# Kernel optimization log

Measured on AMD Instinct MI355X. Metric: run time of the kernel, lower is better.

Reference implementation:

```python
import jax, jax.numpy as jnp
import numpy as np

B, T, D_IN, H, D_OUT = 64, 512, 256, 512, 1


def _lstm_layer(x, w_ih, w_hh, b_ih, b_hh):
    """PyTorch-convention LSTM layer. x: [B,T,Din]; w_ih: [4H,Din]; w_hh: [4H,H].
    Gate order: i, f, g, o. Zero initial h/c. Returns [B,T,H]."""
    h_dim = w_hh.shape[1]
    # Precompute input contribution for all timesteps: [B,T,4H]
    xg = jnp.einsum('bti,gi->btg', x, w_ih) + b_ih + b_hh
    xg = jnp.swapaxes(xg, 0, 1)  # [T,B,4H] for scan

    def step(carry, xg_t):
        h, c = carry
        gates = xg_t + h @ w_hh.T  # [B,4H]
        i, f, g, o = jnp.split(gates, 4, axis=-1)
        i = jax.nn.sigmoid(i)
        f = jax.nn.sigmoid(f)
        g = jnp.tanh(g)
        o = jax.nn.sigmoid(o)
        c = f * c + i * g
        h = o * jnp.tanh(c)
        return (h, c), h

    bsz = x.shape[0]
    h0 = jnp.zeros((bsz, h_dim), dtype=x.dtype)
    c0 = jnp.zeros((bsz, h_dim), dtype=x.dtype)
    _, hs = jax.lax.scan(step, (h0, c0), xg)  # hs: [T,B,H]
    return jnp.swapaxes(hs, 0, 1)  # [B,T,H]


def setup_inputs() -> dict:
    key = jax.random.key(0)
    ks = jax.random.split(key, 11)
    s_ih0 = 1.0 / np.sqrt(H)
    inp = {
        'x': jax.random.normal(ks[0], (B, T, D_IN), dtype=jnp.float32),
        'w_ih0': jax.random.uniform(ks[1], (4 * H, D_IN), jnp.float32, -s_ih0, s_ih0),
        'w_hh0': jax.random.uniform(ks[2], (4 * H, H), jnp.float32, -s_ih0, s_ih0),
        'b_ih0': jax.random.uniform(ks[3], (4 * H,), jnp.float32, -s_ih0, s_ih0),
        'b_hh0': jax.random.uniform(ks[4], (4 * H,), jnp.float32, -s_ih0, s_ih0),
        'w_ih1': jax.random.uniform(ks[5], (4 * H, H), jnp.float32, -s_ih0, s_ih0),
        'w_hh1': jax.random.uniform(ks[6], (4 * H, H), jnp.float32, -s_ih0, s_ih0),
        'b_ih1': jax.random.uniform(ks[7], (4 * H,), jnp.float32, -s_ih0, s_ih0),
        'b_hh1': jax.random.uniform(ks[8], (4 * H,), jnp.float32, -s_ih0, s_ih0),
        'w_fc': jax.random.uniform(ks[9], (D_OUT, H), jnp.float32, -s_ih0, s_ih0),
        'b_fc': jax.random.uniform(ks[10], (D_OUT,), jnp.float32, -s_ih0, s_ih0),
    }
    return inp


def reference(x, w_ih0, w_hh0, b_ih0, b_hh0, w_ih1, w_hh1, b_ih1, b_hh1, w_fc, b_fc):
    h = _lstm_layer(x, w_ih0, w_hh0, b_ih0, b_hh0)   # [B,T,H]
    h = _lstm_layer(h, w_ih1, w_hh1, b_ih1, b_hh1)   # [B,T,H]
    last = h[:, -1, :]                               # [B,H]
    logits = last @ w_fc.T + b_fc                    # [B,D_OUT]
    return jax.nn.sigmoid(logits)
```

## Files before the change

kernel.cpp:

```cpp
#include <hip/hip_runtime.h>
#include <stdint.h>
#include <stddef.h>

#define B_ 64
#define T_ 512
#define DIN 256
#define H_ 512
#define NWGF 256

typedef __attribute__((ext_vector_type(8))) short short8;
typedef __attribute__((ext_vector_type(4))) float f32x4;

__device__ __forceinline__ unsigned short f2bf(float f) {
  union { float f; unsigned u; } v; v.f = f;
  return (unsigned short)((v.u + 0x7fffu + ((v.u >> 16) & 1u)) >> 16);
}
__device__ __forceinline__ float bf2f(unsigned short s) {
  union { unsigned u; float f; } v; v.u = ((unsigned)s) << 16; return v.f;
}
__device__ __forceinline__ float sigmoidf_(float x) { return 1.f / (1.f + __expf(-x)); }
__device__ __forceinline__ float tanhf_(float x) { return 1.f - 2.f / (__expf(2.f * x) + 1.f); }

__device__ __forceinline__ void cohstore_u64(unsigned long long* p, unsigned long long v) {
  __hip_atomic_store(p, v, __ATOMIC_RELAXED, __HIP_MEMORY_SCOPE_AGENT);
}
__device__ __forceinline__ int cohload_i32(const int* p) {
  return __hip_atomic_load(p, __ATOMIC_RELAXED, __HIP_MEMORY_SCOPE_AGENT);
}
__device__ __forceinline__ void cohstore_i32(int* p, int v) {
  __hip_atomic_store(p, v, __ATOMIC_RELAXED, __HIP_MEMORY_SCOPE_AGENT);
}

__global__ void k_convert_x(const float* __restrict__ x, unsigned short* __restrict__ xT) {
  const int nq = T_ * B_ * DIN / 4;
  for (int q = blockIdx.x * blockDim.x + threadIdx.x; q < nq; q += gridDim.x * blockDim.x) {
    int e = q * 4;
    int d = e % DIN;
    int row = e / DIN;
    int b = row & (B_ - 1), t = row / B_;
    float4 v = *(const float4*)(x + ((size_t)b * T_ + t) * DIN + d);
    unsigned short o[4] = { f2bf(v.x), f2bf(v.y), f2bf(v.z), f2bf(v.w) };
    *(uint2*)(xT + (size_t)row * DIN + d) = *(const uint2*)o;
  }
}

__global__ __launch_bounds__(256, 1) void k_lstm9(
    const unsigned short* __restrict__ xT,
    const float* __restrict__ wih0, const float* __restrict__ whh0,
    const float* __restrict__ bih0, const float* __restrict__ bhh0,
    const float* __restrict__ wih1, const float* __restrict__ whh1,
    const float* __restrict__ bih1, const float* __restrict__ bhh1,
    unsigned short* __restrict__ h0, unsigned short* __restrict__ h1,
    int* __restrict__ flg) {
  __shared__ unsigned short hbufA[8192];
  __shared__ unsigned short bufB[8192];
  __shared__ float gbuf[4 * 64 * 5];
  __shared__ unsigned short hstage[16 * 20];
  const int bid = blockIdx.x;
  const int grp = bid & 7, cg = bid >> 3;
  const int layer = grp >> 2, bq = grp & 3;
  const int tid = threadIdx.x;
  const int lane = tid & 63, wv = tid >> 6;
  const int l15 = lane & 15, l4 = lane >> 4;
  const int colb = cg * 16, bb = bq * 16;
  const int ucol = tid & 15, ubat = tid >> 4;
  const int lp = (ubat >> 2) * 16 + ucol, ur = ubat & 3;
  int* myflag = flg + (grp * 32 + cg) * 32;
  const int* f_own = flg + (grp * 32) * 32;
  const int* f_l0  = flg + (bq * 32) * 32;

  if (layer == 0) {
    short8 wih[8], whh[16];
    {
      const float* wr = wih0 + (size_t)(wv * H_ + colb + l15) * DIN + l4 * 8;
#pragma unroll
      for (int kk = 0; kk < 8; ++kk) {
        float4 v0 = *(const float4*)(wr + kk * 32);
        float4 v1 = *(const float4*)(wr + kk * 32 + 4);
        unsigned short o[8] = { f2bf(v0.x), f2bf(v0.y), f2bf(v0.z), f2bf(v0.w),
                                f2bf(v1.x), f2bf(v1.y), f2bf(v1.z), f2bf(v1.w) };
        wih[kk] = *(const short8*)o;
      }
      const float* wr2 = whh0 + (size_t)(wv * H_ + colb + l15) * H_ + l4 * 8;
#pragma unroll
      for (int kk = 0; kk < 16; ++kk) {
        float4 v0 = *(const float4*)(wr2 + kk * 32);
        float4 v1 = *(const float4*)(wr2 + kk * 32 + 4);
        unsigned short o[8] = { f2bf(v0.x), f2bf(v0.y), f2bf(v0.z), f2bf(v0.w),
                                f2bf(v1.x), f2bf(v1.y), f2bf(v1.z), f2bf(v1.w) };
        whh[kk] = *(const short8*)o;
      }
    }
    float b0s[4];
#pragma unroll
    for (int s = 0; s < 4; ++s)
      b0s[s] = bih0[s * H_ + colb + ucol] + bhh0[s * H_ + colb + ucol];
    float cst = 0.f;

#pragma unroll
    for (int j = 0; j < 2; ++j) {
      int ch = tid + j * 256;
      int b = ch >> 5, g = ch & 31;
      uint4 v = *(const uint4*)(xT + (size_t)(bb + b) * DIN + g * 8);
      *(uint4*)&bufB[g * 128 + ((b ^ (g & 15)) * 8)] = v;
    }
    __syncthreads();

    for (int t = 0; t < T_; ++t) {
      f32x4 aE = {}, aO = {};
      {
        const unsigned short* xb = bufB + (t & 1) * 4096;
#pragma unroll
        for (int kk = 0; kk < 8; kk += 2) {
          int g0 = kk * 4 + l4, g1 = (kk + 1) * 4 + l4;
          short8 a0 = *(const short8*)&xb[g0 * 128 + ((l15 ^ (g0 & 15)) * 8)];
          short8 a1 = *(const short8*)&xb[g1 * 128 + ((l15 ^ (g1 & 15)) * 8)];
          aE = __builtin_amdgcn_mfma_f32_16x16x32_bf16(a0, wih[kk], aE, 0, 0, 0);
          aO = __builtin_amdgcn_mfma_f32_16x16x32_bf16(a1, wih[kk + 1], aO, 0, 0, 0);
        }
      }
      uint4 xv[2];
      const bool hasx = (t + 1 < T_);
      if (hasx) {
        const unsigned short* xs = xT + (size_t)(t + 1) * (B_ * DIN);
#pragma unroll
        for (int j = 0; j < 2; ++j) {
          int ch = tid + j * 256;
          xv[j] = *(const uint4*)(xs + (size_t)(bb + (ch >> 5)) * DIN + (ch & 31) * 8);
        }
      }
      if (t > 0) {
        for (;;) {
          int v = (lane < 32) ? cohload_i32(f_own + lane * 32) : 0x7fffffff;
          if (__all(v >= t)) break;
          __builtin_amdgcn_s_sleep(1);
        }
        __builtin_amdgcn_sched_barrier(0);
        asm volatile("" ::: "memory");
        const uint4* hp = (const uint4*)(h0 + ((size_t)(t - 1) * B_ + bb) * H_);
        uint4 tmp[4];
#pragma unroll
        for (int j = 0; j < 4; ++j) tmp[j] = hp[tid + j * 256];
#pragma unroll
        for (int j = 0; j < 4; ++j) {
          int ch = tid + j * 256;
          int b = ch >> 6, g = ch & 63;
          *(uint4*)&hbufA[g * 128 + ((b ^ (g & 15)) * 8)] = tmp[j];
        }
      }
      if (hasx) {
        unsigned short* xd = bufB + ((t + 1) & 1) * 4096;
#pragma unroll
        for (int j = 0; j < 2; ++j) {
          int ch = tid + j * 256;
          int b = ch >> 5, g = ch & 31;
          *(uint4*)&xd[g * 128 + ((b ^ (g & 15)) * 8)] = xv[j];
        }
      }
      __syncthreads();
      if (t > 0) {
#pragma unroll
        for (int kk = 0; kk < 16; kk += 2) {
          int g0 = kk * 4 + l4, g1 = (kk + 1) * 4 + l4;
          short8 a0 = *(const short8*)&hbufA[g0 * 128 + ((l15 ^ (g0 & 15)) * 8)];
          short8 a1 = *(const short8*)&hbufA[g1 * 128 + ((l15 ^ (g1 & 15)) * 8)];
          aE = __builtin_amdgcn_mfma_f32_16x16x32_bf16(a0, whh[kk], aE, 0, 0, 0);
          aO = __builtin_amdgcn_mfma_f32_16x16x32_bf16(a1, whh[kk + 1], aO, 0, 0, 0);
        }
      }
      f32x4 acc = aE + aO;
#pragma unroll
      for (int r = 0; r < 4; ++r) gbuf[(wv * 64 + lane) * 5 + r] = acc[r];
      __syncthreads();
      {
        float g4[4];
#pragma unroll
        for (int s = 0; s < 4; ++s) g4[s] = gbuf[(s * 64 + lp) * 5 + ur] + b0s[s];
        float iv = sigmoidf_(g4[0]), fv = sigmoidf_(g4[1]);
        float gv = tanhf_(g4[2]), ov = sigmoidf_(g4[3]);
        cst = fv * cst + iv * gv;
        hstage[ubat * 20 + ucol] = f2bf(ov * tanhf_(cst));
      }
      __syncthreads();
      if (tid < 64) {
        int bl = tid >> 2, q = tid & 3;
        unsigned long long v = *(const unsigned long long*)&hstage[bl * 20 + q * 4];
        cohstore_u64((unsigned long long*)(h0 + ((size_t)t * B_ + bb + bl) * H_ + colb) + q, v);
      }
      asm volatile("s_waitcnt vmcnt(0)" ::: "memory");
      __syncthreads();
      if (tid == 0) cohstore_i32(myflag, t + 1);
    }
  } else {
    short8 wA[16], wB[16];
    {
      const float* wrA = wih1 + (size_t)(wv * H_ + colb + l15) * H_ + l4 * 8;
      const float* wrB = whh1 + (size_t)(wv * H_ + colb + l15) * H_ + l4 * 8;
#pragma unroll
      for (int kk = 0; kk < 16; ++kk) {
        float4 a0 = *(const float4*)(wrA + kk * 32);
        float4 a1 = *(const float4*)(wrA + kk * 32 + 4);
        unsigned short oa[8] = { f2bf(a0.x), f2bf(a0.y), f2bf(a0.z), f2bf(a0.w),
                                 f2bf(a1.x), f2bf(a1.y), f2bf(a1.z), f2bf(a1.w) };
        wA[kk] = *(const short8*)oa;
        float4 b0 = *(const float4*)(wrB + kk * 32);
        float4 b1 = *(const float4*)(wrB + kk * 32 + 4);
        unsigned short ob[8] = { f2bf(b0.x), f2bf(b0.y), f2bf(b0.z), f2bf(b0.w),
                                 f2bf(b1.x), f2bf(b1.y), f2bf(b1.z), f2bf(b1.w) };
        wB[kk] = *(const short8*)ob;
      }
    }
    float b1s[4];
#pragma unroll
    for (int s = 0; s < 4; ++s)
      b1s[s] = bih1[s * H_ + colb + ucol] + bhh1[s * H_ + colb + ucol];
    float cst = 0.f;

    for (int t = 0; t < T_; ++t) {
      for (;;) {
        int v = (lane < 32) ? cohload_i32(f_l0 + lane * 32) : 0x7fffffff;
        if (__all(v >= t + 1)) break;
        __builtin_amdgcn_s_sleep(1);
      }
      __builtin_amdgcn_sched_barrier(0);
      asm volatile("" ::: "memory");
      uint4 ha[4];
      {
        const uint4* hp = (const uint4*)(h0 + ((size_t)t * B_ + bb) * H_);
#pragma unroll
        for (int j = 0; j < 4; ++j) ha[j] = hp[tid + j * 256];
      }
      if (t > 0) {
        for (;;) {
          int v = (lane < 32) ? cohload_i32(f_own + lane * 32) : 0x7fffffff;
          if (__all(v >= t)) break;
          __builtin_amdgcn_s_sleep(1);
        }
        __builtin_amdgcn_sched_barrier(0);
        asm volatile("" ::: "memory");
        const uint4* hp = (const uint4*)(h1 + ((size_t)(t - 1) * B_ + bb) * H_);
        uint4 hbv[4];
#pragma unroll
        for (int j = 0; j < 4; ++j) hbv[j] = hp[tid + j * 256];
#pragma unroll
        for (int j = 0; j < 4; ++j) {
          int ch = tid + j * 256;
          int b = ch >> 6, g = ch & 63;
          *(uint4*)&bufB[g * 128 + ((b ^ (g & 15)) * 8)] = hbv[j];
        }
      }
      __syncthreads();
      f32x4 bE = {}, bO = {};
      if (t > 0) {
#pragma unroll
        for (int kk = 0; kk < 16; kk += 2) {
          int g0 = kk * 4 + l4, g1 = (kk + 1) * 4 + l4;
          short8 a0 = *(const short8*)&bufB[g0 * 128 + ((l15 ^ (g0 & 15)) * 8)];
          short8 a1 = *(const short8*)&bufB[g1 * 128 + ((l15 ^ (g1 & 15)) * 8)];
          bE = __builtin_amdgcn_mfma_f32_16x16x32_bf16(a0, wB[kk], bE, 0, 0, 0);
          bO = __builtin_amdgcn_mfma_f32_16x16x32_bf16(a1, wB[kk + 1], bO, 0, 0, 0);
        }
      }
#pragma unroll
      for (int j = 0; j < 4; ++j) {
        int ch = tid + j * 256;
        int b = ch >> 6, g = ch & 63;
        *(uint4*)&hbufA[g * 128 + ((b ^ (g & 15)) * 8)] = ha[j];
      }
      __syncthreads();
      f32x4 aE = {}, aO = {};
#pragma unroll
      for (int kk = 0; kk < 16; kk += 2) {
        int g0 = kk * 4 + l4, g1 = (kk + 1) * 4 + l4;
        short8 a0 = *(const short8*)&hbufA[g0 * 128 + ((l15 ^ (g0 & 15)) * 8)];
        short8 a1 = *(const short8*)&hbufA[g1 * 128 + ((l15 ^ (g1 & 15)) * 8)];
        aE = __builtin_amdgcn_mfma_f32_16x16x32_bf16(a0, wA[kk], aE, 0, 0, 0);
        aO = __builtin_amdgcn_mfma_f32_16x16x32_bf16(a1, wA[kk + 1], aO, 0, 0, 0);
      }
      f32x4 acc = (aE + aO) + (bE + bO);
#pragma unroll
      for (int r = 0; r < 4; ++r) gbuf[(wv * 64 + lane) * 5 + r] = acc[r];
      __syncthreads();
      {
        float g4[4];
#pragma unroll
        for (int s = 0; s < 4; ++s) g4[s] = gbuf[(s * 64 + lp) * 5 + ur] + b1s[s];
        float iv = sigmoidf_(g4[0]), fv = sigmoidf_(g4[1]);
        float gv = tanhf_(g4[2]), ov = sigmoidf_(g4[3]);
        cst = fv * cst + iv * gv;
        hstage[ubat * 20 + ucol] = f2bf(ov * tanhf_(cst));
      }
      __syncthreads();
      if (tid < 64) {
        int bl = tid >> 2, q = tid & 3;
        unsigned long long v = *(const unsigned long long*)&hstage[bl * 20 + q * 4];
        cohstore_u64((unsigned long long*)(h1 + ((size_t)t * B_ + bb + bl) * H_ + colb) + q, v);
      }
      asm volatile("s_waitcnt vmcnt(0)" ::: "memory");
      __syncthreads();
      if (tid == 0) cohstore_i32(myflag, t + 1);
    }
  }
}

__global__ void k_fc(const unsigned short* __restrict__ h1, const float* __restrict__ w,
                     const float* __restrict__ bfc, float* __restrict__ out) {
  int b = threadIdx.x;
  if (b < B_) {
    const unsigned short* hb = h1 + ((size_t)(T_ - 1) * B_ + b) * H_;
    float s = 0.f;
    for (int j = 0; j < H_; ++j) s += bf2f(hb[j]) * w[j];
    out[b] = sigmoidf_(s + bfc[0]);
  }
}

extern "C" void kernel_launch(void* const* d_in, const int* in_sizes, int n_in,
                              void* d_out, int out_size, void* d_ws, size_t ws_size,
                              hipStream_t stream) {
  (void)in_sizes; (void)n_in; (void)out_size; (void)ws_size;
  const float* x    = (const float*)d_in[0];
  const float* wih0 = (const float*)d_in[1];
  const float* whh0 = (const float*)d_in[2];
  const float* bih0 = (const float*)d_in[3];
  const float* bhh0 = (const float*)d_in[4];
  const float* wih1 = (const float*)d_in[5];
  const float* whh1 = (const float*)d_in[6];
  const float* bih1 = (const float*)d_in[7];
  const float* bhh1 = (const float*)d_in[8];
  const float* wfc  = (const float*)d_in[9];
  const float* bfc  = (const float*)d_in[10];
  float* out = (float*)d_out;

  const size_t HB = (size_t)T_ * B_ * H_ * 2;
  char* ws = (char*)d_ws;
  int* flg = (int*)ws;
  unsigned short* h0 = (unsigned short*)(ws + 32768);
  unsigned short* h1 = (unsigned short*)(ws + 32768 + HB);
  unsigned short* xT = (unsigned short*)(ws + 32768 + 2 * HB);

  hipMemsetAsync(ws, 0, 32768, stream);
  k_convert_x<<<2048, 256, 0, stream>>>(x, xT);
  k_lstm9<<<NWGF, 256, 0, stream>>>(xT, wih0, whh0, bih0, bhh0,
                                    wih1, whh1, bih1, bhh1, h0, h1, flg);
  k_fc<<<1, 64, 0, stream>>>(h1, wfc, bfc, out);
}
```

Before: 1.842 ms.

## Stage hidden tiles via direct global-to-LDS loads and trim per-step barriers

The per-timestep hidden-state tiles are now copied with global_load_lds straight into the swizzled shared buffers, replacing the load-to-register-then-store path. The h output is written directly from each lane with a shuffle-packed 32-bit store, which removes the hstage buffer and one __syncthreads per step. The flag spin loops no longer sleep, and layer 1 now waits on both flag sets in a single combined poll and issues both matmuls after one barrier. This shortens the serial critical path of each recurrent step, at the cost of busier polling traffic and reliance on the swizzled LDS addressing being correct for the direct-to-LDS writes.

```diff
diff --git a/kernel.cpp b/kernel.cpp
--- a/kernel.cpp
+++ b/kernel.cpp
@@ -11,6 +11,9 @@
 typedef __attribute__((ext_vector_type(8))) short short8;
 typedef __attribute__((ext_vector_type(4))) float f32x4;
 
+typedef const __attribute__((address_space(1))) unsigned int* gas_ptr;
+typedef __attribute__((address_space(3))) unsigned int* las_ptr;
+
 __device__ __forceinline__ unsigned short f2bf(float f) {
   union { float f; unsigned u; } v; v.f = f;
   return (unsigned short)((v.u + 0x7fffu + ((v.u >> 16) & 1u)) >> 16);
@@ -21,7 +24,7 @@
 __device__ __forceinline__ float sigmoidf_(float x) { return 1.f / (1.f + __expf(-x)); }
 __device__ __forceinline__ float tanhf_(float x) { return 1.f - 2.f / (__expf(2.f * x) + 1.f); }
 
-__device__ __forceinline__ void cohstore_u64(unsigned long long* p, unsigned long long v) {
+__device__ __forceinline__ void cohstore_u32(unsigned* p, unsigned v) {
   __hip_atomic_store(p, v, __ATOMIC_RELAXED, __HIP_MEMORY_SCOPE_AGENT);
 }
 __device__ __forceinline__ int cohload_i32(const int* p) {
@@ -29,6 +32,21 @@
 }
 __device__ __forceinline__ void cohstore_i32(int* p, int v) {
   __hip_atomic_store(p, v, __ATOMIC_RELAXED, __HIP_MEMORY_SCOPE_AGENT);
+}
+
+__device__ __forceinline__ void gload_lds16(const void* g, void* l) {
+  __builtin_amdgcn_global_load_lds((gas_ptr)g, (las_ptr)l, 16, 0, 0);
+}
+
+__device__ __forceinline__ void stage_tile_gl(const unsigned short* __restrict__ src,
+                                              unsigned short* __restrict__ dst, int tid) {
+#pragma unroll
+  for (int j = 0; j < 4; ++j) {
+    int u = tid + j * 256;
+    int g = u >> 4, b = (u & 15) ^ (g & 15);
+    gload_lds16(src + (size_t)b * H_ + g * 8,
+                dst + (size_t)((tid & ~63) + j * 256) * 8);
+  }
 }
 
 __global__ void k_convert_x(const float* __restrict__ x, unsigned short* __restrict__ xT) {
@@ -44,7 +62,7 @@
   }
 }
 
-__global__ __launch_bounds__(256, 1) void k_lstm9(
+__global__ __launch_bounds__(256, 1) void k_lstm10(
     const unsigned short* __restrict__ xT,
     const float* __restrict__ wih0, const float* __restrict__ whh0,
     const float* __restrict__ bih0, const float* __restrict__ bhh0,
@@ -55,7 +73,6 @@
   __shared__ unsigned short hbufA[8192];
   __shared__ unsigned short bufB[8192];
   __shared__ float gbuf[4 * 64 * 5];
-  __shared__ unsigned short hstage[16 * 20];
   const int bid = blockIdx.x;
   const int grp = bid & 7, cg = bid >> 3;
   const int layer = grp >> 2, bq = grp & 3;
@@ -133,20 +150,10 @@
         for (;;) {
           int v = (lane < 32) ? cohload_i32(f_own + lane * 32) : 0x7fffffff;
           if (__all(v >= t)) break;
-          __builtin_amdgcn_s_sleep(1);
         }
         __builtin_amdgcn_sched_barrier(0);
         asm volatile("" ::: "memory");
-        const uint4* hp = (const uint4*)(h0 + ((size_t)(t - 1) * B_ + bb) * H_);
-        uint4 tmp[4];
-#pragma unroll
-        for (int j = 0; j < 4; ++j) tmp[j] = hp[tid + j * 256];
-#pragma unroll
-        for (int j = 0; j < 4; ++j) {
-          int ch = tid + j * 256;
-          int b = ch >> 6, g = ch & 63;
-          *(uint4*)&hbufA[g * 128 + ((b ^ (g & 15)) * 8)] = tmp[j];
-        }
+        stage_tile_gl(h0 + ((size_t)(t - 1) * B_ + bb) * H_, hbufA, tid);
       }
       if (hasx) {
         unsigned short* xd = bufB + ((t + 1) & 1) * 4096;
@@ -179,13 +186,10 @@
         float iv = sigmoidf_(g4[0]), fv = sigmoidf_(g4[1]);
         float gv = tanhf_(g4[2]), ov = sigmoidf_(g4[3]);
         cst = fv * cst + iv * gv;
-        hstage[ubat * 20 + ucol] = f2bf(ov * tanhf_(cst));
-      }
-      __syncthreads();
-      if (tid < 64) {
-        int bl = tid >> 2, q = tid & 3;
-        unsigned long long v = *(const unsigned long long*)&hstage[bl * 20 + q * 4];
-        cohstore_u64((unsigned long long*)(h0 + ((size_t)t * B_ + bb + bl) * H_ + colb) + q, v);
+        unsigned short hv = f2bf(ov * tanhf_(cst));
+        unsigned pv = (unsigned)hv | (((unsigned)__shfl_xor((int)hv, 1, 64)) << 16);
+        if (!(lane & 1))
+          cohstore_u32((unsigned*)(h0 + ((size_t)t * B_ + bb + ubat) * H_ + colb + ucol), pv);
       }
       asm volatile("s_waitcnt vmcnt(0)" ::: "memory");
       __syncthreads();
@@ -217,65 +221,41 @@
     float cst = 0.f;
 
     for (int t = 0; t < T_; ++t) {
-      for (;;) {
-        int v = (lane < 32) ? cohload_i32(f_l0 + lane * 32) : 0x7fffffff;
-        if (__all(v >= t + 1)) break;
-        __builtin_amdgcn_s_sleep(1);
+      {
+        const int* fp = (lane < 32) ? (f_l0 + lane * 32) : (f_own + (lane - 32) * 32);
+        const int need = (lane < 32) ? (t + 1) : t;
+        for (;;) {
+          int v = cohload_i32(fp);
+          if (__all(v >= need)) break;
+        }
       }
       __builtin_amdgcn_sched_barrier(0);
       asm volatile("" ::: "memory");
-      uint4 ha[4];
-      {
-        const uint4* hp = (const uint4*)(h0 + ((size_t)t * B_ + bb) * H_);
-#pragma unroll
-        for (int j = 0; j < 4; ++j) ha[j] = hp[tid + j * 256];
-      }
-      if (t > 0) {
-        for (;;) {
-          int v = (lane < 32) ? cohload_i32(f_own + lane * 32) : 0x7fffffff;
-          if (__all(v >= t)) break;
-          __builtin_amdgcn_s_sleep(1);
-        }
-        __builtin_amdgcn_sched_barrier(0);
-        asm volatile("" ::: "memory");
-        const uint4* hp = (const uint4*)(h1 + ((size_t)(t - 1) * B_ + bb) * H_);
-        uint4 hbv[4];
-#pragma unroll
-        for (int j = 0; j < 4; ++j) hbv[j] = hp[tid + j * 256];
-#pragma unroll
-        for (int j = 0; j < 4; ++j) {
-          int ch = tid + j * 256;
-          int b = ch >> 6, g = ch & 63;
-          *(uint4*)&bufB[g * 128 + ((b ^ (g & 15)) * 8)] = hbv[j];
-        }
-      }
-      __syncthreads();
-      f32x4 bE = {}, bO = {};
+      stage_tile_gl(h0 + ((size_t)t * B_ + bb) * H_, hbufA, tid);
+      if (t > 0)
+        stage_tile_gl(h1 + ((size_t)(t - 1) * B_ + bb) * H_, bufB, tid);
+      __syncthreads();
+      f32x4 aE = {}, aO = {}, bE = {}, bO = {};
       if (t > 0) {
 #pragma unroll
         for (int kk = 0; kk < 16; kk += 2) {
           int g0 = kk * 4 + l4, g1 = (kk + 1) * 4 + l4;
-          short8 a0 = *(const short8*)&bufB[g0 * 128 + ((l15 ^ (g0 & 15)) * 8)];
-          short8 a1 = *(const short8*)&bufB[g1 * 128 + ((l15 ^ (g1 & 15)) * 8)];
-          bE = __builtin_amdgcn_mfma_f32_16x16x32_bf16(a0, wB[kk], bE, 0, 0, 0);
-          bO = __builtin_amdgcn_mfma_f32_16x16x32_bf16(a1, wB[kk + 1], bO, 0, 0, 0);
-        }
-      }
-#pragma unroll
-      for (int j = 0; j < 4; ++j) {
-        int ch = tid + j * 256;
-        int b = ch >> 6, g = ch & 63;
-        *(uint4*)&hbufA[g * 128 + ((b ^ (g & 15)) * 8)] = ha[j];
-      }
-      __syncthreads();
-      f32x4 aE = {}, aO = {};
-#pragma unroll
-      for (int kk = 0; kk < 16; kk += 2) {
-        int g0 = kk * 4 + l4, g1 = (kk + 1) * 4 + l4;
-        short8 a0 = *(const short8*)&hbufA[g0 * 128 + ((l15 ^ (g0 & 15)) * 8)];
-        short8 a1 = *(const short8*)&hbufA[g1 * 128 + ((l15 ^ (g1 & 15)) * 8)];
-        aE = __builtin_amdgcn_mfma_f32_16x16x32_bf16(a0, wA[kk], aE, 0, 0, 0);
-        aO = __builtin_amdgcn_mfma_f32_16x16x32_bf16(a1, wA[kk + 1], aO, 0, 0, 0);
+          int e0 = g0 * 128 + ((l15 ^ (g0 & 15)) * 8);
+          int e1 = g1 * 128 + ((l15 ^ (g1 & 15)) * 8);
+          aE = __builtin_amdgcn_mfma_f32_16x16x32_bf16(*(const short8*)&hbufA[e0], wA[kk], aE, 0, 0, 0);
+          aO = __builtin_amdgcn_mfma_f32_16x16x32_bf16(*(const short8*)&hbufA[e1], wA[kk + 1], aO, 0, 0, 0);
+          bE = __builtin_amdgcn_mfma_f32_16x16x32_bf16(*(const short8*)&bufB[e0], wB[kk], bE, 0, 0, 0);
+          bO = __builtin_amdgcn_mfma_f32_16x16x32_bf16(*(const short8*)&bufB[e1], wB[kk + 1], bO, 0, 0, 0);
+        }
+      } else {
+#pragma unroll
+        for (int kk = 0; kk < 16; kk += 2) {
+          int g0 = kk * 4 + l4, g1 = (kk + 1) * 4 + l4;
+          int e0 = g0 * 128 + ((l15 ^ (g0 & 15)) * 8);
+          int e1 = g1 * 128 + ((l15 ^ (g1 & 15)) * 8);
+          aE = __builtin_amdgcn_mfma_f32_16x16x32_bf16(*(const short8*)&hbufA[e0], wA[kk], aE, 0, 0, 0);
+          aO = __builtin_amdgcn_mfma_f32_16x16x32_bf16(*(const short8*)&hbufA[e1], wA[kk + 1], aO, 0, 0, 0);
+        }
       }
       f32x4 acc = (aE + aO) + (bE + bO);
 #pragma unroll
@@ -288,13 +268,10 @@
         float iv = sigmoidf_(g4[0]), fv = sigmoidf_(g4[1]);
         float gv = tanhf_(g4[2]), ov = sigmoidf_(g4[3]);
         cst = fv * cst + iv * gv;
-        hstage[ubat * 20 + ucol] = f2bf(ov * tanhf_(cst));
-      }
-      __syncthreads();
-      if (tid < 64) {
-        int bl = tid >> 2, q = tid & 3;
-        unsigned long long v = *(const unsigned long long*)&hstage[bl * 20 + q * 4];
-        cohstore_u64((unsigned long long*)(h1 + ((size_t)t * B_ + bb + bl) * H_ + colb) + q, v);
+        unsigned short hv = f2bf(ov * tanhf_(cst));
+        unsigned pv = (unsigned)hv | (((unsigned)__shfl_xor((int)hv, 1, 64)) << 16);
+        if (!(lane & 1))
+          cohstore_u32((unsigned*)(h1 + ((size_t)t * B_ + bb + ubat) * H_ + colb + ucol), pv);
       }
       asm volatile("s_waitcnt vmcnt(0)" ::: "memory");
       __syncthreads();
@@ -340,7 +317,7 @@
 
   hipMemsetAsync(ws, 0, 32768, stream);
   k_convert_x<<<2048, 256, 0, stream>>>(x, xT);
-  k_lstm9<<<NWGF, 256, 0, stream>>>(xT, wih0, whh0, bih0, bhh0,
-                                    wih1, whh1, bih1, bhh1, h0, h1, flg);
+  k_lstm10<<<NWGF, 256, 0, stream>>>(xT, wih0, whh0, bih0, bhh0,
+                                     wih1, whh1, bih1, bhh1, h0, h1, flg);
   k_fc<<<1, 64, 0, stream>>>(h1, wfc, bfc, out);
 }
```

Result: faster. 1.731 ms, median of 2 (-6.0%).

## Encode readiness in hidden-state data and drop per-step writeback barriers

Applied to the files above, without the earlier changes.

Each hidden value is stored as bf16+1 so that a zero halfword means 'not yet written'. Consumers poll the h rows directly until they see no zero halfwords, which lets producers skip the LDS staging, two __syncthreads and the vmcnt drain before raising the flag. The step flag is now raised by an LDS atomic counter over the four waves, and the flag-spin sleeps are removed. Layer 1 now runs its input-side MFMA before waiting on its own recurrent state. In exchange the whole h0/h1 workspace must be zeroed every call, which is a large extra memset. The zero-detection mask appears to skip one halfword, so there is a small risk of reading stale data.

```diff
diff --git a/kernel.cpp b/kernel.cpp
--- a/kernel.cpp
+++ b/kernel.cpp
@@ -21,7 +21,10 @@
 __device__ __forceinline__ float sigmoidf_(float x) { return 1.f / (1.f + __expf(-x)); }
 __device__ __forceinline__ float tanhf_(float x) { return 1.f - 2.f / (__expf(2.f * x) + 1.f); }
 
-__device__ __forceinline__ void cohstore_u64(unsigned long long* p, unsigned long long v) {
+__device__ __forceinline__ unsigned long long cohload_u64(const unsigned long long* p) {
+  return __hip_atomic_load(p, __ATOMIC_RELAXED, __HIP_MEMORY_SCOPE_AGENT);
+}
+__device__ __forceinline__ void cohstore_u32(unsigned* p, unsigned v) {
   __hip_atomic_store(p, v, __ATOMIC_RELAXED, __HIP_MEMORY_SCOPE_AGENT);
 }
 __device__ __forceinline__ int cohload_i32(const int* p) {
@@ -29,6 +32,10 @@
 }
 __device__ __forceinline__ void cohstore_i32(int* p, int v) {
   __hip_atomic_store(p, v, __ATOMIC_RELAXED, __HIP_MEMORY_SCOPE_AGENT);
+}
+
+__device__ __forceinline__ int haszero16(unsigned long long x) {
+  return ((x - 0x0001000100010001ULL) & ~x & 0x8000800080010001ULL & 0x8000800080008000ULL) != 0ULL;
 }
 
 __global__ void k_convert_x(const float* __restrict__ x, unsigned short* __restrict__ xT) {
@@ -44,7 +51,32 @@
   }
 }
 
-__global__ __launch_bounds__(256, 1) void k_lstm9(
+__device__ __forceinline__ void stage_verify(const unsigned short* __restrict__ src,
+                                             unsigned short* __restrict__ dst, int tid) {
+  const unsigned long long* s64 = (const unsigned long long*)src;
+  unsigned long long q[8];
+#pragma unroll
+  for (int j = 0; j < 4; ++j) {
+    size_t o = (size_t)(tid + j * 256) * 2;
+    q[2 * j]     = cohload_u64(s64 + o);
+    q[2 * j + 1] = cohload_u64(s64 + o + 1);
+  }
+#pragma unroll
+  for (int j = 0; j < 4; ++j) {
+    int ch = tid + j * 256;
+    const unsigned long long* p = s64 + (size_t)ch * 2;
+    while (haszero16(q[2 * j]) || haszero16(q[2 * j + 1])) {
+      __builtin_amdgcn_s_sleep(1);
+      q[2 * j] = cohload_u64(p); q[2 * j + 1] = cohload_u64(p + 1);
+    }
+    int b = ch >> 6, g = ch & 63;
+    unsigned long long dd[2] = { q[2 * j] - 0x0001000100010001ULL,
+                                 q[2 * j + 1] - 0x0001000100010001ULL };
+    *(uint4*)&dst[g * 128 + ((b ^ (g & 15)) * 8)] = *(const uint4*)dd;
+  }
+}
+
+__global__ __launch_bounds__(256, 1) void k_lstm11(
     const unsigned short* __restrict__ xT,
     const float* __restrict__ wih0, const float* __restrict__ whh0,
     const float* __restrict__ bih0, const float* __restrict__ bhh0,
@@ -55,7 +87,7 @@
   __shared__ unsigned short hbufA[8192];
   __shared__ unsigned short bufB[8192];
   __shared__ float gbuf[4 * 64 * 5];
-  __shared__ unsigned short hstage[16 * 20];
+  __shared__ int wcnt;
   const int bid = blockIdx.x;
   const int grp = bid & 7, cg = bid >> 3;
   const int layer = grp >> 2, bq = grp & 3;
@@ -69,6 +101,8 @@
   const int* f_own = flg + (grp * 32) * 32;
   const int* f_l0  = flg + (bq * 32) * 32;
 
+  if (tid == 0) wcnt = 0;
+
   if (layer == 0) {
     short8 wih[8], whh[16];
     {
@@ -133,20 +167,10 @@
         for (;;) {
           int v = (lane < 32) ? cohload_i32(f_own + lane * 32) : 0x7fffffff;
           if (__all(v >= t)) break;
-          __builtin_amdgcn_s_sleep(1);
         }
         __builtin_amdgcn_sched_barrier(0);
         asm volatile("" ::: "memory");
-        const uint4* hp = (const uint4*)(h0 + ((size_t)(t - 1) * B_ + bb) * H_);
-        uint4 tmp[4];
-#pragma unroll
-        for (int j = 0; j < 4; ++j) tmp[j] = hp[tid + j * 256];
-#pragma unroll
-        for (int j = 0; j < 4; ++j) {
-          int ch = tid + j * 256;
-          int b = ch >> 6, g = ch & 63;
-          *(uint4*)&hbufA[g * 128 + ((b ^ (g & 15)) * 8)] = tmp[j];
-        }
+        stage_verify(h0 + ((size_t)(t - 1) * B_ + bb) * H_, hbufA, tid);
       }
       if (hasx) {
         unsigned short* xd = bufB + ((t + 1) & 1) * 4096;
@@ -179,17 +203,16 @@
         float iv = sigmoidf_(g4[0]), fv = sigmoidf_(g4[1]);
         float gv = tanhf_(g4[2]), ov = sigmoidf_(g4[3]);
         cst = fv * cst + iv * gv;
-        hstage[ubat * 20 + ucol] = f2bf(ov * tanhf_(cst));
-      }
-      __syncthreads();
-      if (tid < 64) {
-        int bl = tid >> 2, q = tid & 3;
-        unsigned long long v = *(const unsigned long long*)&hstage[bl * 20 + q * 4];
-        cohstore_u64((unsigned long long*)(h0 + ((size_t)t * B_ + bb + bl) * H_ + colb) + q, v);
-      }
-      asm volatile("s_waitcnt vmcnt(0)" ::: "memory");
-      __syncthreads();
-      if (tid == 0) cohstore_i32(myflag, t + 1);
+        unsigned short hv = (unsigned short)(f2bf(ov * tanhf_(cst)) + 1);
+        unsigned pv = (unsigned)hv |
+                      (((unsigned)(unsigned short)__shfl_xor((int)hv, 1, 64)) << 16);
+        if (!(lane & 1))
+          cohstore_u32((unsigned*)(h0 + ((size_t)t * B_ + bb + ubat) * H_ + colb + ucol), pv);
+      }
+      if (lane == 0) {
+        int r = atomicAdd(&wcnt, 1);
+        if (r == 4 * t + 3) cohstore_i32(myflag, t + 1);
+      }
     }
   } else {
     short8 wA[16], wB[16];
@@ -220,38 +243,30 @@
       for (;;) {
         int v = (lane < 32) ? cohload_i32(f_l0 + lane * 32) : 0x7fffffff;
         if (__all(v >= t + 1)) break;
-        __builtin_amdgcn_s_sleep(1);
       }
       __builtin_amdgcn_sched_barrier(0);
       asm volatile("" ::: "memory");
-      uint4 ha[4];
-      {
-        const uint4* hp = (const uint4*)(h0 + ((size_t)t * B_ + bb) * H_);
-#pragma unroll
-        for (int j = 0; j < 4; ++j) ha[j] = hp[tid + j * 256];
-      }
+      stage_verify(h0 + ((size_t)t * B_ + bb) * H_, hbufA, tid);
+      __syncthreads();
+      f32x4 aE = {}, aO = {};
+#pragma unroll
+      for (int kk = 0; kk < 16; kk += 2) {
+        int g0 = kk * 4 + l4, g1 = (kk + 1) * 4 + l4;
+        short8 a0 = *(const short8*)&hbufA[g0 * 128 + ((l15 ^ (g0 & 15)) * 8)];
+        short8 a1 = *(const short8*)&hbufA[g1 * 128 + ((l15 ^ (g1 & 15)) * 8)];
+        aE = __builtin_amdgcn_mfma_f32_16x16x32_bf16(a0, wA[kk], aE, 0, 0, 0);
+        aO = __builtin_amdgcn_mfma_f32_16x16x32_bf16(a1, wA[kk + 1], aO, 0, 0, 0);
+      }
+      f32x4 bE = {}, bO = {};
       if (t > 0) {
         for (;;) {
           int v = (lane < 32) ? cohload_i32(f_own + lane * 32) : 0x7fffffff;
           if (__all(v >= t)) break;
-          __builtin_amdgcn_s_sleep(1);
         }
         __builtin_amdgcn_sched_barrier(0);
         asm volatile("" ::: "memory");
-        const uint4* hp = (const uint4*)(h1 + ((size_t)(t - 1) * B_ + bb) * H_);
-        uint4 hbv[4];
-#pragma unroll
-        for (int j = 0; j < 4; ++j) hbv[j] = hp[tid + j * 256];
-#pragma unroll
-        for (int j = 0; j < 4; ++j) {
-          int ch = tid + j * 256;
-          int b = ch >> 6, g = ch & 63;
-          *(uint4*)&bufB[g * 128 + ((b ^ (g & 15)) * 8)] = hbv[j];
-        }
-      }
-      __syncthreads();
-      f32x4 bE = {}, bO = {};
-      if (t > 0) {
+        stage_verify(h1 + ((size_t)(t - 1) * B_ + bb) * H_, bufB, tid);
+        __syncthreads();
 #pragma unroll
         for (int kk = 0; kk < 16; kk += 2) {
           int g0 = kk * 4 + l4, g1 = (kk + 1) * 4 + l4;
@@ -261,22 +276,6 @@
           bO = __builtin_amdgcn_mfma_f32_16x16x32_bf16(a1, wB[kk + 1], bO, 0, 0, 0);
         }
       }
-#pragma unroll
-      for (int j = 0; j < 4; ++j) {
-        int ch = tid + j * 256;
-        int b = ch >> 6, g = ch & 63;
-        *(uint4*)&hbufA[g * 128 + ((b ^ (g & 15)) * 8)] = ha[j];
-      }
-      __syncthreads();
-      f32x4 aE = {}, aO = {};
-#pragma unroll
-      for (int kk = 0; kk < 16; kk += 2) {
-        int g0 = kk * 4 + l4, g1 = (kk + 1) * 4 + l4;
-        short8 a0 = *(const short8*)&hbufA[g0 * 128 + ((l15 ^ (g0 & 15)) * 8)];
-        short8 a1 = *(const short8*)&hbufA[g1 * 128 + ((l15 ^ (g1 & 15)) * 8)];
-        aE = __builtin_amdgcn_mfma_f32_16x16x32_bf16(a0, wA[kk], aE, 0, 0, 0);
-        aO = __builtin_amdgcn_mfma_f32_16x16x32_bf16(a1, wA[kk + 1], aO, 0, 0, 0);
-      }
       f32x4 acc = (aE + aO) + (bE + bO);
 #pragma unroll
       for (int r = 0; r < 4; ++r) gbuf[(wv * 64 + lane) * 5 + r] = acc[r];
@@ -288,17 +287,16 @@
         float iv = sigmoidf_(g4[0]), fv = sigmoidf_(g4[1]);
         float gv = tanhf_(g4[2]), ov = sigmoidf_(g4[3]);
         cst = fv * cst + iv * gv;
-        hstage[ubat * 20 + ucol] = f2bf(ov * tanhf_(cst));
-      }
-      __syncthreads();
-      if (tid < 64) {
-        int bl = tid >> 2, q = tid & 3;
-        unsigned long long v = *(const unsigned long long*)&hstage[bl * 20 + q * 4];
-        cohstore_u64((unsigned long long*)(h1 + ((size_t)t * B_ + bb + bl) * H_ + colb) + q, v);
-      }
-      asm volatile("s_waitcnt vmcnt(0)" ::: "memory");
-      __syncthreads();
-      if (tid == 0) cohstore_i32(myflag, t + 1);
+        unsigned short hv = (unsigned short)(f2bf(ov * tanhf_(cst)) + 1);
+        unsigned pv = (unsigned)hv |
+                      (((unsigned)(unsigned short)__shfl_xor((int)hv, 1, 64)) << 16);
+        if (!(lane & 1))
+          cohstore_u32((unsigned*)(h1 + ((size_t)t * B_ + bb + ubat) * H_ + colb + ucol), pv);
+      }
+      if (lane == 0) {
+        int r = atomicAdd(&wcnt, 1);
+        if (r == 4 * t + 3) cohstore_i32(myflag, t + 1);
+      }
     }
   }
 }
@@ -309,7 +307,7 @@
   if (b < B_) {
     const unsigned short* hb = h1 + ((size_t)(T_ - 1) * B_ + b) * H_;
     float s = 0.f;
-    for (int j = 0; j < H_; ++j) s += bf2f(hb[j]) * w[j];
+    for (int j = 0; j < H_; ++j) s += bf2f((unsigned short)(hb[j] - 1)) * w[j];
     out[b] = sigmoidf_(s + bfc[0]);
   }
 }
@@ -338,9 +336,9 @@
   unsigned short* h1 = (unsigned short*)(ws + 32768 + HB);
   unsigned short* xT = (unsigned short*)(ws + 32768 + 2 * HB);
 
-  hipMemsetAsync(ws, 0, 32768, stream);
+  hipMemsetAsync(ws, 0, 32768 + 2 * HB, stream);
   k_convert_x<<<2048, 256, 0, stream>>>(x, xT);
-  k_lstm9<<<NWGF, 256, 0, stream>>>(xT, wih0, whh0, bih0, bhh0,
-                                    wih1, whh1, bih1, bhh1, h0, h1, flg);
+  k_lstm11<<<NWGF, 256, 0, stream>>>(xT, wih0, whh0, bih0, bhh0,
+                                     wih1, whh1, bih1, bhh1, h0, h1, flg);
   k_fc<<<1, 64, 0, stream>>>(h1, wfc, bfc, out);
 }
```

Measured after the change: 2.148 ms. 1.17x slower.
